# Optimization experiments

Measured on AMD Instinct MI355X. Metric: run time of the kernel, lower is better.

## Reference

```python
import jax, jax.numpy as jnp
import numpy as np


def _pairwise_sqdist(a, b):
    # a: [B,N,3], b: [B,M,3] -> [B,N,M] squared L2 distances
    a2 = jnp.sum(a * a, axis=-1)            # [B,N]
    b2 = jnp.sum(b * b, axis=-1)            # [B,M]
    ab = jnp.einsum('bnd,bmd->bnm', a, b)   # [B,N,M]
    d = a2[:, :, None] + b2[:, None, :] - 2.0 * ab
    return jnp.maximum(d, 0.0)


def setup_inputs() -> dict:
    key = jax.random.key(0)
    k1, k2 = jax.random.split(key)
    B, N, M = 4, 8192, 8192
    p1 = jax.random.normal(k1, (B, N, 3), dtype=jnp.float32)
    p2 = jax.random.normal(k2, (B, M, 3), dtype=jnp.float32)
    return {"p1": p1, "p2": p2}


def reference(p1, p2):
    # chamfer_3DDist: squared L2 NN distances both directions, then mean of each
    d = _pairwise_sqdist(p1, p2)   # [B,N,M]
    d1 = jnp.min(d, axis=2)        # [B,N] nearest p2 for each p1 point
    d2 = jnp.min(d, axis=1)        # [B,M] nearest p1 for each p2 point
    return jnp.mean(d1) + jnp.mean(d2)
```

## Files before the change

### kernel.cpp

```cpp
#include <hip/hip_runtime.h>
#include <float.h>


#define BLK   256
#define QPT   4
#define QPB   (BLK * QPT)
#define BATCH 4
#define NPTS  8192
#define NCH   16
#define CHUNK (NPTS / NCH)
#define QTILES (NPTS / QPB)
#define GRID  (2 * BATCH * QTILES * NCH)
#define TOTQ  (2 * BATCH * NPTS)

__global__ __launch_bounds__(BLK) void init_kernel(unsigned* mins, float* out, int n) {
    int i = blockIdx.x * BLK + threadIdx.x;
    if (i < n) mins[i] = 0x7F7FFFFFu;
    if (i == 0) out[0] = 0.f;
}

__global__ __launch_bounds__(BLK) void cd_chunk_kernel(
    const float* __restrict__ p1, const float* __restrict__ p2,
    unsigned* __restrict__ mins)
{
    __shared__ float4 pts[CHUNK];
    int bid    = blockIdx.x;
    int mchunk = bid & (NCH - 1);
    int qt     = (bid >> 4) & (QTILES - 1);
    int batch  = (bid >> 7) & (BATCH - 1);
    int dir    = bid >> 9;

    const float* qbase = (dir == 0 ? p1 : p2) + (size_t)batch * NPTS * 3;
    const float* dbase = (dir == 0 ? p2 : p1) + (size_t)batch * NPTS * 3;

    int tid = threadIdx.x;

    if (tid < CHUNK / 4) {
        int t4 = tid * 4;
        const float* s = dbase + (size_t)(mchunk * CHUNK + t4) * 3;
        float4 f0 = *(const float4*)(s);
        float4 f1 = *(const float4*)(s + 4);
        float4 f2 = *(const float4*)(s + 8);
        float x0 = f0.x, y0 = f0.y, z0 = f0.z;
        float x1 = f0.w, y1 = f1.x, z1 = f1.y;
        float x2 = f1.z, y2 = f1.w, z2 = f2.x;
        float x3 = f2.y, y3 = f2.z, z3 = f2.w;
        pts[t4 + 0] = make_float4(x0, y0, z0, -0.5f * (x0*x0 + y0*y0 + z0*z0));
        pts[t4 + 1] = make_float4(x1, y1, z1, -0.5f * (x1*x1 + y1*y1 + z1*z1));
        pts[t4 + 2] = make_float4(x2, y2, z2, -0.5f * (x2*x2 + y2*y2 + z2*z2));
        pts[t4 + 3] = make_float4(x3, y3, z3, -0.5f * (x3*x3 + y3*y3 + z3*z3));
    }

    float qx[QPT], qy[QPT], qz[QPT], qn[QPT];
    #pragma unroll
    for (int k = 0; k < QPT; ++k) {
        int q = qt * QPB + k * BLK + tid;
        const float* s = qbase + (size_t)q * 3;
        qx[k] = s[0]; qy[k] = s[1]; qz[k] = s[2];
        qn[k] = qx[k] * qx[k] + qy[k] * qy[k] + qz[k] * qz[k];
    }
    __syncthreads();

    float s0[QPT], s1[QPT];
    #pragma unroll
    for (int k = 0; k < QPT; ++k) { s0[k] = -FLT_MAX; s1[k] = -FLT_MAX; }

    float4 c0 = pts[0], c1 = pts[1], c2 = pts[2], c3 = pts[3];
    #pragma unroll 2
    for (int j = 0; j < CHUNK - 4; j += 4) {
        float4 n0 = pts[j + 4];
        float4 n1 = pts[j + 5];
        float4 n2 = pts[j + 6];
        float4 n3 = pts[j + 7];
        #pragma unroll
        for (int k = 0; k < QPT; ++k) {
            float d0 = fmaf(qz[k], c0.z, fmaf(qy[k], c0.y, fmaf(qx[k], c0.x, c0.w)));
            float d1 = fmaf(qz[k], c1.z, fmaf(qy[k], c1.y, fmaf(qx[k], c1.x, c1.w)));
            float d2 = fmaf(qz[k], c2.z, fmaf(qy[k], c2.y, fmaf(qx[k], c2.x, c2.w)));
            float d3 = fmaf(qz[k], c3.z, fmaf(qy[k], c3.y, fmaf(qx[k], c3.x, c3.w)));
            s0[k] = fmaxf(s0[k], fmaxf(d0, d1));
            s1[k] = fmaxf(s1[k], fmaxf(d2, d3));
        }
        c0 = n0; c1 = n1; c2 = n2; c3 = n3;
    }
    #pragma unroll
    for (int k = 0; k < QPT; ++k) {
        float d0 = fmaf(qz[k], c0.z, fmaf(qy[k], c0.y, fmaf(qx[k], c0.x, c0.w)));
        float d1 = fmaf(qz[k], c1.z, fmaf(qy[k], c1.y, fmaf(qx[k], c1.x, c1.w)));
        float d2 = fmaf(qz[k], c2.z, fmaf(qy[k], c2.y, fmaf(qx[k], c2.x, c2.w)));
        float d3 = fmaf(qz[k], c3.z, fmaf(qy[k], c3.y, fmaf(qx[k], c3.x, c3.w)));
        s0[k] = fmaxf(s0[k], fmaxf(d0, d1));
        s1[k] = fmaxf(s1[k], fmaxf(d2, d3));
    }

    unsigned qid = (unsigned)(dir * (BATCH * NPTS) + batch * NPTS + qt * QPB + tid);
    #pragma unroll
    for (int k = 0; k < QPT; ++k) {
        float d = fmaxf(qn[k] - 2.f * fmaxf(s0[k], s1[k]), 0.f);
        atomicMin(&mins[qid + k * BLK], __float_as_uint(d));
    }
}

__global__ __launch_bounds__(BLK) void sum_kernel(
    const unsigned* __restrict__ mins, float* __restrict__ out, int n, float scale)
{
    int i = blockIdx.x * BLK + threadIdx.x;
    int stride = gridDim.x * BLK;
    float v = 0.f;
    for (int idx = i; idx < n; idx += stride) v += __uint_as_float(mins[idx]);
    for (int off = 32; off > 0; off >>= 1) v += __shfl_down(v, off, 64);
    __shared__ float wsum[BLK / 64];
    int lane = threadIdx.x & 63, wid = threadIdx.x >> 6;
    if (lane == 0) wsum[wid] = v;
    __syncthreads();
    if (threadIdx.x == 0) {
        float t = 0.f;
        for (int w = 0; w < BLK / 64; ++w) t += wsum[w];
        atomicAdd(out, t * scale);
    }
}

__global__ void zero_out_kernel(float* out) { out[0] = 0.f; }

__global__ __launch_bounds__(BLK) void cd_full_kernel(
    const float* __restrict__ p1, const float* __restrict__ p2,
    float* __restrict__ out)
{
    __shared__ float4 pts[2048];
    int bid   = blockIdx.x;
    int qt    = bid & 15;
    int batch = (bid >> 4) & 3;
    int dir   = bid >> 6;

    const float* qbase = (dir == 0 ? p1 : p2) + (size_t)batch * NPTS * 3;
    const float* dbase = (dir == 0 ? p2 : p1) + (size_t)batch * NPTS * 3;

    int tid = threadIdx.x;
    int q0 = qt * 512 + tid;
    int q1 = q0 + BLK;
    float ax = qbase[q0 * 3 + 0], ay = qbase[q0 * 3 + 1], az = qbase[q0 * 3 + 2];
    float bx = qbase[q1 * 3 + 0], by = qbase[q1 * 3 + 1], bz = qbase[q1 * 3 + 2];
    float an = ax * ax + ay * ay + az * az;
    float bn = bx * bx + by * by + bz * bz;

    float sa = -FLT_MAX, sb = -FLT_MAX;
    for (int c = 0; c < 4; ++c) {
        __syncthreads();
        int mstart = c * 2048;
        for (int j = tid; j < 2048; j += BLK) {
            const float* s = dbase + (size_t)(mstart + j) * 3;
            float x = s[0], y = s[1], z = s[2];
            pts[j] = make_float4(x, y, z, -0.5f * (x * x + y * y + z * z));
        }
        __syncthreads();
        #pragma unroll 4
        for (int j = 0; j < 2048; j += 2) {
            float4 u = pts[j];
            float4 v = pts[j + 1];
            float s;
            s = fmaf(ax, u.x, u.w); s = fmaf(ay, u.y, s); s = fmaf(az, u.z, s); sa = fmaxf(sa, s);
            s = fmaf(bx, u.x, u.w); s = fmaf(by, u.y, s); s = fmaf(bz, u.z, s); sb = fmaxf(sb, s);
            s = fmaf(ax, v.x, v.w); s = fmaf(ay, v.y, s); s = fmaf(az, v.z, s); sa = fmaxf(sa, s);
            s = fmaf(bx, v.x, v.w); s = fmaf(by, v.y, s); s = fmaf(bz, v.z, s); sb = fmaxf(sb, s);
        }
    }
    float da = fmaxf(an - 2.f * sa, 0.f);
    float db = fmaxf(bn - 2.f * sb, 0.f);
    float v = da + db;
    for (int off = 32; off > 0; off >>= 1) v += __shfl_down(v, off, 64);
    __shared__ float wsum[BLK / 64];
    int lane = threadIdx.x & 63, wid = threadIdx.x >> 6;
    if (lane == 0) wsum[wid] = v;
    __syncthreads();
    if (threadIdx.x == 0) {
        float t = 0.f;
        for (int w = 0; w < BLK / 64; ++w) t += wsum[w];
        atomicAdd(out, t * (1.f / (float)(BATCH * NPTS)));
    }
}

extern "C" void kernel_launch(void* const* d_in, const int* in_sizes, int n_in,
                              void* d_out, int out_size, void* d_ws, size_t ws_size,
                              hipStream_t stream) {
    const float* p1 = (const float*)d_in[0];
    const float* p2 = (const float*)d_in[1];
    float* out = (float*)d_out;

    if (ws_size >= (size_t)TOTQ * sizeof(unsigned)) {
        unsigned* mins = (unsigned*)d_ws;
        init_kernel<<<TOTQ / BLK, BLK, 0, stream>>>(mins, out, TOTQ);
        cd_chunk_kernel<<<GRID, BLK, 0, stream>>>(p1, p2, mins);
        sum_kernel<<<64, BLK, 0, stream>>>(mins, out, TOTQ, 1.f / (float)(BATCH * NPTS));
    } else {
        zero_out_kernel<<<1, 1, 0, stream>>>(out);
        cd_full_kernel<<<128, BLK, 0, stream>>>(p1, p2, out);
    }
}
```

Before: 98.52 us.

## Pack candidate points in paired SoA layout to use packed FP32 FMA

Rearranges the shared-memory candidate tile so that each pair of points stores x, y, z and w as adjacent two-wide vectors. The inner loop then uses two-wide elementwise FMA, which is meant to map to packed FP32 FMA instructions on CDNA and halve the FMA instruction count. The cost is extra unpacking and max operations per pair, and it relies on the compiler actually emitting packed instructions. The register-level prefetch of the next candidates is also removed.

```diff
diff --git a/kernel.cpp b/kernel.cpp
--- a/kernel.cpp
+++ b/kernel.cpp
@@ -1,6 +1,8 @@
 #include <hip/hip_runtime.h>
 #include <float.h>
 
+
+typedef float v2f __attribute__((ext_vector_type(2)));
 
 #define BLK   256
 #define QPT   4
@@ -45,58 +47,61 @@
         float x1 = f0.w, y1 = f1.x, z1 = f1.y;
         float x2 = f1.z, y2 = f1.w, z2 = f2.x;
         float x3 = f2.y, y3 = f2.z, z3 = f2.w;
-        pts[t4 + 0] = make_float4(x0, y0, z0, -0.5f * (x0*x0 + y0*y0 + z0*z0));
-        pts[t4 + 1] = make_float4(x1, y1, z1, -0.5f * (x1*x1 + y1*y1 + z1*z1));
-        pts[t4 + 2] = make_float4(x2, y2, z2, -0.5f * (x2*x2 + y2*y2 + z2*z2));
-        pts[t4 + 3] = make_float4(x3, y3, z3, -0.5f * (x3*x3 + y3*y3 + z3*z3));
-    }
-
-    float qx[QPT], qy[QPT], qz[QPT], qn[QPT];
+        float w0 = -0.5f * (x0*x0 + y0*y0 + z0*z0);
+        float w1 = -0.5f * (x1*x1 + y1*y1 + z1*z1);
+        float w2 = -0.5f * (x2*x2 + y2*y2 + z2*z2);
+        float w3 = -0.5f * (x3*x3 + y3*y3 + z3*z3);
+        pts[4*tid + 0] = make_float4(x0, x1, y0, y1);
+        pts[4*tid + 1] = make_float4(z0, z1, w0, w1);
+        pts[4*tid + 2] = make_float4(x2, x3, y2, y3);
+        pts[4*tid + 3] = make_float4(z2, z3, w2, w3);
+    }
+
+    v2f qx2[QPT], qy2[QPT], qz2[QPT];
+    float qn[QPT];
     #pragma unroll
     for (int k = 0; k < QPT; ++k) {
         int q = qt * QPB + k * BLK + tid;
         const float* s = qbase + (size_t)q * 3;
-        qx[k] = s[0]; qy[k] = s[1]; qz[k] = s[2];
-        qn[k] = qx[k] * qx[k] + qy[k] * qy[k] + qz[k] * qz[k];
+        float qx = s[0], qy = s[1], qz = s[2];
+        qx2[k] = (v2f){qx, qx};
+        qy2[k] = (v2f){qy, qy};
+        qz2[k] = (v2f){qz, qz};
+        qn[k] = qx * qx + qy * qy + qz * qz;
     }
     __syncthreads();
 
-    float s0[QPT], s1[QPT];
+    float acc0[QPT], acc1[QPT];
     #pragma unroll
-    for (int k = 0; k < QPT; ++k) { s0[k] = -FLT_MAX; s1[k] = -FLT_MAX; }
-
-    float4 c0 = pts[0], c1 = pts[1], c2 = pts[2], c3 = pts[3];
+    for (int k = 0; k < QPT; ++k) { acc0[k] = -FLT_MAX; acc1[k] = -FLT_MAX; }
+
     #pragma unroll 2
-    for (int j = 0; j < CHUNK - 4; j += 4) {
-        float4 n0 = pts[j + 4];
-        float4 n1 = pts[j + 5];
-        float4 n2 = pts[j + 6];
-        float4 n3 = pts[j + 7];
+    for (int m = 0; m < CHUNK / 2; m += 2) {
+        float4 u0 = pts[2*m + 0];
+        float4 v0 = pts[2*m + 1];
+        float4 u1 = pts[2*m + 2];
+        float4 v1 = pts[2*m + 3];
+        v2f X0 = (v2f){u0.x, u0.y}, Y0 = (v2f){u0.z, u0.w};
+        v2f Z0 = (v2f){v0.x, v0.y}, W0 = (v2f){v0.z, v0.w};
+        v2f X1 = (v2f){u1.x, u1.y}, Y1 = (v2f){u1.z, u1.w};
+        v2f Z1 = (v2f){v1.x, v1.y}, W1 = (v2f){v1.z, v1.w};
         #pragma unroll
         for (int k = 0; k < QPT; ++k) {
-            float d0 = fmaf(qz[k], c0.z, fmaf(qy[k], c0.y, fmaf(qx[k], c0.x, c0.w)));
-            float d1 = fmaf(qz[k], c1.z, fmaf(qy[k], c1.y, fmaf(qx[k], c1.x, c1.w)));
-            float d2 = fmaf(qz[k], c2.z, fmaf(qy[k], c2.y, fmaf(qx[k], c2.x, c2.w)));
-            float d3 = fmaf(qz[k], c3.z, fmaf(qy[k], c3.y, fmaf(qx[k], c3.x, c3.w)));
-            s0[k] = fmaxf(s0[k], fmaxf(d0, d1));
-            s1[k] = fmaxf(s1[k], fmaxf(d2, d3));
+            v2f s0 = __builtin_elementwise_fma(qz2[k], Z0,
+                      __builtin_elementwise_fma(qy2[k], Y0,
+                       __builtin_elementwise_fma(qx2[k], X0, W0)));
+            acc0[k] = fmaxf(acc0[k], fmaxf(s0.x, s0.y));
+            v2f s1 = __builtin_elementwise_fma(qz2[k], Z1,
+                      __builtin_elementwise_fma(qy2[k], Y1,
+                       __builtin_elementwise_fma(qx2[k], X1, W1)));
+            acc1[k] = fmaxf(acc1[k], fmaxf(s1.x, s1.y));
         }
-        c0 = n0; c1 = n1; c2 = n2; c3 = n3;
-    }
-    #pragma unroll
-    for (int k = 0; k < QPT; ++k) {
-        float d0 = fmaf(qz[k], c0.z, fmaf(qy[k], c0.y, fmaf(qx[k], c0.x, c0.w)));
-        float d1 = fmaf(qz[k], c1.z, fmaf(qy[k], c1.y, fmaf(qx[k], c1.x, c1.w)));
-        float d2 = fmaf(qz[k], c2.z, fmaf(qy[k], c2.y, fmaf(qx[k], c2.x, c2.w)));
-        float d3 = fmaf(qz[k], c3.z, fmaf(qy[k], c3.y, fmaf(qx[k], c3.x, c3.w)));
-        s0[k] = fmaxf(s0[k], fmaxf(d0, d1));
-        s1[k] = fmaxf(s1[k], fmaxf(d2, d3));
     }
 
     unsigned qid = (unsigned)(dir * (BATCH * NPTS) + batch * NPTS + qt * QPB + tid);
     #pragma unroll
     for (int k = 0; k < QPT; ++k) {
-        float d = fmaxf(qn[k] - 2.f * fmaxf(s0[k], s1[k]), 0.f);
+        float d = fmaxf(qn[k] - 2.f * fmaxf(acc0[k], acc1[k]), 0.f);
         atomicMin(&mins[qid + k * BLK], __float_as_uint(d));
     }
 }
```

Measured after the change: 98.16 us. No clear change (-0.4%).
